# Kernel optimization log

Hardware: AMD Instinct MI355X
Metric: run time of the kernel (lower is better)

## Reference

```python
import jax, jax.numpy as jnp
import numpy as np

B, OBS, ACT, NT, E = 4096, 512, 64, 10, 16
DREP, DH, DK = 1024, 1024, 512  # rep dim, expert hidden, key/value dim


def setup_inputs() -> dict:
    key = jax.random.key(0)
    ks = jax.random.split(key, 24)
    s = 0.02
    state_core = jax.random.normal(ks[0], (B, OBS), jnp.float32)
    task_ids = jax.random.randint(ks[1], (B,), 0, NT)
    onehot = jax.nn.one_hot(task_ids, NT, dtype=jnp.float32)
    state = jnp.concatenate([state_core, onehot], axis=-1)  # [B, OBS+NT]
    act = jax.random.normal(ks[2], (B, ACT), jnp.float32)
    return {
        "state": state,
        "act": act,
        "rep_W0": s * jax.random.normal(ks[3], (OBS + ACT, DREP), jnp.float32),
        "rep_b0": jnp.zeros((DREP,), jnp.float32),
        "rep_W1": s * jax.random.normal(ks[4], (DREP, DREP), jnp.float32),
        "rep_b1": jnp.zeros((DREP,), jnp.float32),
        "emb": 0.5 * jnp.ones((NT, DK), jnp.float32),
        "Wk0": s * jax.random.normal(ks[5], (E, DREP, DH), jnp.float32),
        "bk0": jnp.zeros((E, DH), jnp.float32),
        "Wk1": s * jax.random.normal(ks[6], (E, DH, DK), jnp.float32),
        "bk1": jnp.zeros((E, DK), jnp.float32),
        "Wv0": s * jax.random.normal(ks[7], (E, DREP, DH), jnp.float32),
        "bv0": jnp.zeros((E, DH), jnp.float32),
        "Wv1": s * jax.random.normal(ks[8], (E, DH, DK), jnp.float32),
        "bv1": jnp.zeros((E, DK), jnp.float32),
        "Wt0": s * jax.random.normal(ks[9], (DK, 512), jnp.float32),
        "bt0": jnp.zeros((512,), jnp.float32),
        "Wt1": s * jax.random.normal(ks[10], (512, 256), jnp.float32),
        "bt1": jnp.zeros((256,), jnp.float32),
        "Wt2": s * jax.random.normal(ks[11], (256, 1), jnp.float32),
        "bt2": jnp.zeros((1,), jnp.float32),
    }


def reference(state, act, rep_W0, rep_b0, rep_W1, rep_b1, emb,
              Wk0, bk0, Wk1, bk1, Wv0, bv0, Wv1, bv1,
              Wt0, bt0, Wt1, bt1, Wt2, bt2):
    num_tasks = emb.shape[0]
    task = jnp.argmax(state[:, -num_tasks:], axis=-1)  # one-hot -> index (== torch.nonzero)
    s = state[:, :-num_tasks]
    # representation: mlp([obs+act, 1024, 1024]) -> relu then identity
    x = jnp.concatenate([s, act], axis=-1)
    rep = jax.nn.relu(x @ rep_W0 + rep_b0) @ rep_W1 + rep_b1  # [B, DREP]
    query = jnp.tanh(emb[task])  # [B, DK]
    # all experts batched (original loops in Python over E tiny MLPs)
    hk = jax.nn.relu(jnp.einsum('bd,edh->ebh', rep, Wk0) + bk0[:, None, :])
    keys = jnp.einsum('ebh,ehk->ebk', hk, Wk1) + bk1[:, None, :]   # [E,B,DK]
    hv = jax.nn.relu(jnp.einsum('bd,edh->ebh', rep, Wv0) + bv0[:, None, :])
    vals = jnp.einsum('ebh,ehk->ebk', hv, Wv1) + bv1[:, None, :]   # [E,B,DK]
    logits = jnp.einsum('bk,ebk->be', query, keys)                 # [B,E]
    attn = jax.nn.softmax(logits, axis=1)
    tower_in = jnp.einsum('be,ebk->bk', attn, vals)                # [B,DK]
    h = jax.nn.relu(tower_in @ Wt0 + bt0)
    h = jax.nn.relu(h @ Wt1 + bt1)
    q = jnp.squeeze(h @ Wt2 + bt2, -1)                             # [B]
    expert_loss = -jnp.mean(
        jnp.sum(jnp.clip(jnp.log(attn + 1e-10), -6.0, 0.0), axis=-1) * 0.3)
    return q, expert_loss
```

## Files before the change

kernel.cpp:

```cpp
#include <hip/hip_runtime.h>
#include <cstdint>
#include <cstddef>

#define NB   4096
#define OBS  512
#define NACT 64
#define NT   10
#define NE   16
#define DREP 1024
#define DH   1024
#define DK   512
#define SLD  (OBS + NT)
#define XK   (OBS + NACT)

typedef short s8v __attribute__((ext_vector_type(8)));
typedef float f4v __attribute__((ext_vector_type(4)));

__device__ __forceinline__ unsigned short f2bf(float f) {
  union { float f; unsigned int u; } v; v.f = f;
  unsigned int u = v.u;
  unsigned int r = (u + 0x7FFFu + ((u >> 16) & 1u)) >> 16;
  return (unsigned short)r;
}
__device__ __forceinline__ float bf2f(unsigned short h) {
  union { unsigned int u; float f; } v; v.u = ((unsigned int)h) << 16;
  return v.f;
}

__device__ __forceinline__ void gload_lds16(const unsigned short* gp, const unsigned short* lp) {
  __builtin_amdgcn_global_load_lds(
      (const __attribute__((address_space(1))) void*)(uintptr_t)gp,
      (__attribute__((address_space(3))) void*)(unsigned int)(uintptr_t)lp,
      16, 0, 0);
}

template <int BM, int BN, int MODE, int RELU, int LDA, int LDB, int KK>
__global__ void __launch_bounds__(256)
gemm_k(const unsigned short* __restrict__ A,
       const unsigned short* __restrict__ Bt,
       const float* __restrict__ bias,
       unsigned short* __restrict__ outB, int ldo,
       const float* __restrict__ qk1, const int* __restrict__ task,
       float* __restrict__ logits, int eBase,
       const float* __restrict__ attn, float* __restrict__ cio)
{
  constexpr int FM = BM / 32;
  constexpr int FN = BN / 32;
  constexpr int CA = BM / 64;
  constexpr int CB = BN / 64;
  constexpr int NTILES = KK / 32;
  static_assert(NTILES >= 3, "pipeline depth");
  constexpr int LPS = CA + CB;
  static_assert(LPS < 16, "vmcnt immediate fits in low bits");
  constexpr int WAIT_STAGE = 0xF70 | LPS;
  constexpr int WAIT_ALL   = 0xF70;

  __shared__ __align__(16) unsigned short As[3][BM * 32];
  __shared__ __align__(16) unsigned short Bs[3][BN * 32];

  const int tid  = threadIdx.x;
  const int wave = tid >> 6;
  const int lane = tid & 63;
  const int wm = wave >> 1, wn = wave & 1;

  const int rowBase = blockIdx.x * BM;
  const int colBase = blockIdx.y * BN;

  int eg = 0;
  if (MODE == 1) {
    eg = blockIdx.z;
    Bt  += (size_t)eg * (DREP * DH);
    bias += eg * DH;
    qk1 += (size_t)eg * (NT * DH);
  }
  if (MODE == 2) {
    eg = eBase + blockIdx.z;
    Bt  += (size_t)eg * (DREP * DH);
    bias += eg * DH;
    outB += (size_t)blockIdx.z * DH;
  }
  if (MODE == 3 || MODE == 4) {
    A   += (size_t)blockIdx.z * KK;
    Bt  += (size_t)blockIdx.z * KK;
    cio += (size_t)blockIdx.z * NB * DK;
  }

  f4v acc[FM][FN];
#pragma unroll
  for (int m = 0; m < FM; ++m)
#pragma unroll
    for (int n = 0; n < FN; ++n) acc[m][n] = f4v{0.f, 0.f, 0.f, 0.f};

  const int sRow = lane >> 2;
  const int sSw  = ((lane & 3) ^ ((sRow >> 1) & 3)) * 8;

  const unsigned short* ag[CA];
  const unsigned short* bg[CB];
#pragma unroll
  for (int j = 0; j < CA; ++j)
    ag[j] = A + (size_t)(rowBase + (wave * CA + j) * 16 + sRow) * LDA + sSw;
#pragma unroll
  for (int j = 0; j < CB; ++j)
    bg[j] = Bt + (size_t)(colBase + (wave * CB + j) * 16 + sRow) * LDB + sSw;

  const int fr   = lane & 15;
  const int koSw = ((lane >> 4) ^ ((fr >> 1) & 3)) * 8;
  const int aOff = (wm * (BM / 2) + fr) * 32 + koSw;
  const int bOff = (wn * (BN / 2) + fr) * 32 + koSw;

  auto stage = [&](int buf) {
#pragma unroll
    for (int j = 0; j < CA; ++j) { gload_lds16(ag[j], &As[buf][(wave * CA + j) * 512]); ag[j] += 32; }
#pragma unroll
    for (int j = 0; j < CB; ++j) { gload_lds16(bg[j], &Bs[buf][(wave * CB + j) * 512]); bg[j] += 32; }
  };

  auto compute = [&](int buf) {
    s8v av[FM], bv[FN];
#pragma unroll
    for (int m = 0; m < FM; ++m)
      av[m] = *reinterpret_cast<const s8v*>(&As[buf][aOff + m * 512]);
#pragma unroll
    for (int n = 0; n < FN; ++n)
      bv[n] = *reinterpret_cast<const s8v*>(&Bs[buf][bOff + n * 512]);
#pragma unroll
    for (int m = 0; m < FM; ++m)
#pragma unroll
      for (int n = 0; n < FN; ++n)
        acc[m][n] = __builtin_amdgcn_mfma_f32_16x16x32_bf16(av[m], bv[n], acc[m][n], 0, 0, 0);
  };

  stage(0);
  stage(1);

  for (int t = 0; t < NTILES; t += 3) {
    if (t + 1 < NTILES) __builtin_amdgcn_s_waitcnt(WAIT_STAGE);
    else                __builtin_amdgcn_s_waitcnt(WAIT_ALL);
    __builtin_amdgcn_s_barrier();
    if (t + 2 < NTILES) stage(2);
    compute(0);
    if (t + 1 < NTILES) {
      if (t + 2 < NTILES) __builtin_amdgcn_s_waitcnt(WAIT_STAGE);
      else                __builtin_amdgcn_s_waitcnt(WAIT_ALL);
      __builtin_amdgcn_s_barrier();
      if (t + 3 < NTILES) stage(0);
      compute(1);
    }
    if (t + 2 < NTILES) {
      if (t + 3 < NTILES) __builtin_amdgcn_s_waitcnt(WAIT_STAGE);
      else                __builtin_amdgcn_s_waitcnt(WAIT_ALL);
      __builtin_amdgcn_s_barrier();
      if (t + 4 < NTILES) stage(1);
      compute(2);
    }
  }

  const int cr = (lane >> 4) * 4;
  const int cc = lane & 15;

  int gcn[FN];
  float bcol[FN];
#pragma unroll
  for (int n = 0; n < FN; ++n) {
    gcn[n] = colBase + wn * (BN / 2) + n * 16 + cc;
    bcol[n] = (MODE >= 3) ? 0.f : bias[gcn[n]];
  }

  if (MODE == 0 || MODE == 2) {
#pragma unroll
    for (int m = 0; m < FM; ++m)
#pragma unroll
      for (int r = 0; r < 4; ++r) {
        int gr = rowBase + wm * (BM / 2) + m * 16 + cr + r;
        float aw = 1.f;
        if (MODE == 2) aw = attn[gr * NE + eg];
#pragma unroll
        for (int n = 0; n < FN; ++n) {
          float v = acc[m][n][r] + bcol[n];
          if (RELU) v = fmaxf(v, 0.f);
          if (MODE == 2) v *= aw;
          outB[(size_t)gr * ldo + gcn[n]] = f2bf(v);
        }
      }
  }

  if (MODE == 1) {
#pragma unroll
    for (int m = 0; m < FM; ++m)
#pragma unroll
      for (int r = 0; r < 4; ++r) {
        int gr = rowBase + wm * (BM / 2) + m * 16 + cr + r;
        int tk = task[gr];
        const float* qrow = qk1 + (size_t)tk * DH;
        float s = 0.f;
#pragma unroll
        for (int n = 0; n < FN; ++n) {
          float v = fmaxf(acc[m][n][r] + bcol[n], 0.f);
          s += v * qrow[gcn[n]];
        }
#pragma unroll
        for (int off = 1; off < 16; off <<= 1) s += __shfl_xor(s, off, 64);
        if (cc == 0) atomicAdd(&logits[gr * NE + eg], s);
      }
  }

  if (MODE == 3 || MODE == 4) {
#pragma unroll
    for (int m = 0; m < FM; ++m)
#pragma unroll
      for (int r = 0; r < 4; ++r) {
        int gr = rowBase + wm * (BM / 2) + m * 16 + cr + r;
#pragma unroll
        for (int n = 0; n < FN; ++n) {
          float v = acc[m][n][r];
          if (MODE == 4) v += cio[(size_t)gr * DK + gcn[n]];
          cio[(size_t)gr * DK + gcn[n]] = v;
        }
      }
  }
}

__global__ void task_k(const float* __restrict__ state, int* __restrict__ task) {
  int b = blockIdx.x * blockDim.x + threadIdx.x;
  if (b >= NB) return;
  const float* p = state + (size_t)b * SLD + OBS;
  float best = p[0]; int bi = 0;
  for (int j = 1; j < NT; ++j) { float v = p[j]; if (v > best) { best = v; bi = j; } }
  task[b] = bi;
}

__global__ void buildx_k(const float* __restrict__ state, const float* __restrict__ act,
                         unsigned short* __restrict__ x) {
  int idx = blockIdx.x * blockDim.x + threadIdx.x;
  if (idx >= NB * XK) return;
  int b = idx / XK, j = idx - b * XK;
  float v = (j < OBS) ? state[(size_t)b * SLD + j] : act[(size_t)b * NACT + (j - OBS)];
  x[idx] = f2bf(v);
}

__global__ void prep_emb_k(const float* __restrict__ emb, const float* __restrict__ bk1,
                           float* __restrict__ Qt, float* __restrict__ qb) {
  int t = blockIdx.x;
  __shared__ float qsh[DK];
  for (int k = threadIdx.x; k < DK; k += 256) {
    float v = tanhf(emb[t * DK + k]);
    Qt[t * DK + k] = v;
    qsh[k] = v;
  }
  __syncthreads();
  int wave = threadIdx.x >> 6, lane = threadIdx.x & 63;
  for (int e = wave; e < NE; e += 4) {
    float s = 0.f;
    for (int k = lane; k < DK; k += 64) s += qsh[k] * bk1[e * DK + k];
    for (int off = 1; off < 64; off <<= 1) s += __shfl_xor(s, off, 64);
    if (lane == 0) qb[e * NT + t] = s;
  }
}

__global__ void qk1_k(const float* __restrict__ Wk1, const float* __restrict__ Qt,
                      float* __restrict__ qk1) {
  int w = (blockIdx.x * blockDim.x + threadIdx.x) >> 6;
  int lane = threadIdx.x & 63;
  if (w >= NE * DH) return;
  int e = w >> 10, h = w & (DH - 1);
  const float* wrow = Wk1 + ((size_t)e * DH + h) * DK + lane * 8;
  float wv[8];
#pragma unroll
  for (int j = 0; j < 8; ++j) wv[j] = wrow[j];
#pragma unroll
  for (int t = 0; t < NT; ++t) {
    const float* qrow = Qt + t * DK + lane * 8;
    float s = 0.f;
#pragma unroll
    for (int j = 0; j < 8; ++j) s += wv[j] * qrow[j];
#pragma unroll
    for (int off = 1; off < 64; off <<= 1) s += __shfl_xor(s, off, 64);
    if (lane == 0) qk1[((size_t)e * NT + t) * DH + h] = s;
  }
}

__global__ void __launch_bounds__(256)
convT_k(const float* __restrict__ src, unsigned short* __restrict__ dst,
        int N, long sBS, long dBS, int dLd) {
  __shared__ float tile[64][65];
  int e = blockIdx.z;
  int n0 = blockIdx.x * 64, k0 = blockIdx.y * 64;
  src += (size_t)e * sBS + (size_t)k0 * N + n0;
  dst += (size_t)e * dBS + (size_t)n0 * dLd + k0;
  int t = threadIdx.x;
  int c4 = t & 15, kr = t >> 4;
#pragma unroll
  for (int i = 0; i < 4; ++i) {
    float4 v = *(const float4*)(src + (size_t)(kr + i * 16) * N + c4 * 4);
    tile[kr + i * 16][c4 * 4 + 0] = v.x;
    tile[kr + i * 16][c4 * 4 + 1] = v.y;
    tile[kr + i * 16][c4 * 4 + 2] = v.z;
    tile[kr + i * 16][c4 * 4 + 3] = v.w;
  }
  __syncthreads();
  int sub = t & 7, nl = t >> 3;
#pragma unroll
  for (int pass = 0; pass < 2; ++pass) {
    int n = nl + pass * 32;
    unsigned short v8[8];
#pragma unroll
    for (int j = 0; j < 8; ++j) v8[j] = f2bf(tile[sub * 8 + j][n]);
    *reinterpret_cast<s8v*>(dst + (size_t)n * dLd + sub * 8) =
        *reinterpret_cast<const s8v*>(v8);
  }
}

__global__ void softmax_k(const float* __restrict__ logits, const float* __restrict__ qb,
                          const int* __restrict__ task, float* __restrict__ attn,
                          float* __restrict__ lossOut) {
  int b = blockIdx.x * blockDim.x + threadIdx.x;
  int t = task[b];
  float l[NE];
  float mx = -1e30f;
#pragma unroll
  for (int e = 0; e < NE; ++e) { l[e] = logits[b * NE + e] + qb[e * NT + t]; mx = fmaxf(mx, l[e]); }
  float s = 0.f;
#pragma unroll
  for (int e = 0; e < NE; ++e) { l[e] = expf(l[e] - mx); s += l[e]; }
  float inv = 1.f / s;
  float loss = 0.f;
#pragma unroll
  for (int e = 0; e < NE; ++e) {
    float a = l[e] * inv;
    attn[b * NE + e] = a;
    float lg = logf(a + 1e-10f);
    loss += fminf(fmaxf(lg, -6.f), 0.f);
  }
  for (int off = 1; off < 64; off <<= 1) loss += __shfl_xor(loss, off, 64);
  if ((threadIdx.x & 63) == 0) atomicAdd(lossOut, loss * (-0.3f / NB));
}

__global__ void towerbias_k(const float* __restrict__ attn, const float* __restrict__ bv1,
                            float* __restrict__ towerin) {
  int idx = blockIdx.x * blockDim.x + threadIdx.x;
  if (idx >= NB * DK) return;
  int b = idx >> 9, k = idx & (DK - 1);
  float s = 0.f;
#pragma unroll
  for (int e = 0; e < NE; ++e) s += attn[b * NE + e] * bv1[e * DK + k];
  towerin[idx] = s;
}

__global__ void cvt_ti_k(const float* __restrict__ twin, const float* __restrict__ P,
                         unsigned short* __restrict__ ti) {
  int idx = (blockIdx.x * blockDim.x + threadIdx.x) * 8;
  if (idx >= NB * DK) return;
  float v[8];
#pragma unroll
  for (int j = 0; j < 8; ++j) v[j] = twin[idx + j];
#pragma unroll
  for (int c = 0; c < 4; ++c) {
    const float* p = P + (size_t)c * NB * DK + idx;
#pragma unroll
    for (int j = 0; j < 8; ++j) v[j] += p[j];
  }
  unsigned short v8[8];
#pragma unroll
  for (int j = 0; j < 8; ++j) v8[j] = f2bf(v[j]);
  *reinterpret_cast<s8v*>(ti + idx) = *reinterpret_cast<const s8v*>(v8);
}

__global__ void qfinal_k(const unsigned short* __restrict__ h2, const float* __restrict__ Wt2,
                         const float* __restrict__ bt2, float* __restrict__ out) {
  int w = (blockIdx.x * blockDim.x + threadIdx.x) >> 6;
  int lane = threadIdx.x & 63;
  if (w >= NB) return;
  float s = 0.f;
#pragma unroll
  for (int j = 0; j < 4; ++j) {
    int k = lane * 4 + j;
    s += bf2f(h2[(size_t)w * 256 + k]) * Wt2[k];
  }
  for (int off = 1; off < 64; off <<= 1) s += __shfl_xor(s, off, 64);
  if (lane == 0) out[w] = s + bt2[0];
}

extern "C" void kernel_launch(void* const* d_in, const int* in_sizes, int n_in,
                              void* d_out, int out_size, void* d_ws, size_t ws_size,
                              hipStream_t stream) {
  const float* state  = (const float*)d_in[0];
  const float* act    = (const float*)d_in[1];
  const float* rep_W0 = (const float*)d_in[2];
  const float* rep_b0 = (const float*)d_in[3];
  const float* rep_W1 = (const float*)d_in[4];
  const float* rep_b1 = (const float*)d_in[5];
  const float* emb    = (const float*)d_in[6];
  const float* Wk0    = (const float*)d_in[7];
  const float* bk0    = (const float*)d_in[8];
  const float* Wk1    = (const float*)d_in[9];
  const float* bk1    = (const float*)d_in[10];
  const float* Wv0    = (const float*)d_in[11];
  const float* bv0    = (const float*)d_in[12];
  const float* Wv1    = (const float*)d_in[13];
  const float* bv1    = (const float*)d_in[14];
  const float* Wt0    = (const float*)d_in[15];
  const float* bt0    = (const float*)d_in[16];
  const float* Wt1    = (const float*)d_in[17];
  const float* bt1    = (const float*)d_in[18];
  const float* Wt2    = (const float*)d_in[19];
  const float* bt2    = (const float*)d_in[20];
  float* out = (float*)d_out;

  char* wsb = (char*)d_ws;
  size_t off = 0;
  auto alloc = [&](size_t bytes) -> void* {
    void* p = wsb + off;
    off += (bytes + 255) & ~(size_t)255;
    return p;
  };
  unsigned short* Ap    = (unsigned short*)alloc((size_t)NB * 8192 * 2);
  unsigned short* Wk0t  = (unsigned short*)alloc((size_t)NE * DREP * DH * 2);
  unsigned short* Wv0t  = (unsigned short*)alloc((size_t)NE * DREP * DH * 2);
  unsigned short* Wv1t  = (unsigned short*)alloc((size_t)DK * (NE * DH) * 2);
  float*          P     = (float*)alloc((size_t)4 * NB * DK * 4);
  unsigned short* h0    = (unsigned short*)alloc((size_t)NB * DREP * 2);
  unsigned short* rep   = (unsigned short*)alloc((size_t)NB * DREP * 2);
  float*          twin  = (float*)alloc((size_t)NB * DK * 4);
  unsigned short* xbuf  = (unsigned short*)alloc((size_t)NB * XK * 2);
  unsigned short* ti    = (unsigned short*)alloc((size_t)NB * DK * 2);
  unsigned short* h1    = (unsigned short*)alloc((size_t)NB * 512 * 2);
  unsigned short* h2    = (unsigned short*)alloc((size_t)NB * 256 * 2);
  unsigned short* rW1t  = (unsigned short*)alloc((size_t)DREP * DREP * 2);
  unsigned short* rW0t  = (unsigned short*)alloc((size_t)DREP * XK * 2);
  float*          qk1   = (float*)alloc((size_t)NE * NT * DH * 4);
  unsigned short* Wt0t  = (unsigned short*)alloc((size_t)512 * 512 * 2);
  unsigned short* Wt1t  = (unsigned short*)alloc((size_t)256 * 512 * 2);
  float*          logits= (float*)alloc((size_t)NB * NE * 4);
  float*          attn  = (float*)alloc((size_t)NB * NE * 4);
  float*          Qt    = (float*)alloc((size_t)NT * DK * 4);
  int*            task  = (int*)alloc((size_t)NB * 4);
  float*          qb    = (float*)alloc((size_t)NE * NT * 4);

  hipMemsetAsync(logits, 0, (size_t)NB * NE * 4, stream);
  hipMemsetAsync(out + NB, 0, sizeof(float), stream);

  task_k<<<NB / 256, 256, 0, stream>>>(state, task);
  buildx_k<<<(NB * XK + 255) / 256, 256, 0, stream>>>(state, act, xbuf);
  prep_emb_k<<<NT, 256, 0, stream>>>(emb, bk1, Qt, qb);
  qk1_k<<<NE * DH / 4, 256, 0, stream>>>(Wk1, Qt, qk1);

  convT_k<<<dim3(DREP / 64, XK / 64, 1), 256, 0, stream>>>(rep_W0, rW0t, DREP, 0, 0, XK);
  convT_k<<<dim3(DREP / 64, DREP / 64, 1), 256, 0, stream>>>(rep_W1, rW1t, DREP, 0, 0, DREP);
  convT_k<<<dim3(DH / 64, DREP / 64, NE), 256, 0, stream>>>(Wk0, Wk0t, DH, (long)DREP * DH, (long)DREP * DH, DREP);
  convT_k<<<dim3(DH / 64, DREP / 64, NE), 256, 0, stream>>>(Wv0, Wv0t, DH, (long)DREP * DH, (long)DREP * DH, DREP);
  convT_k<<<dim3(DK / 64, DH / 64, NE), 256, 0, stream>>>(Wv1, Wv1t, DK, (long)DH * DK, 1024L, NE * DH);
  convT_k<<<dim3(512 / 64, 512 / 64, 1), 256, 0, stream>>>(Wt0, Wt0t, 512, 0, 0, 512);
  convT_k<<<dim3(256 / 64, 512 / 64, 1), 256, 0, stream>>>(Wt1, Wt1t, 256, 0, 0, 512);

  gemm_k<128, 128, 0, 1, XK, XK, XK><<<dim3(NB / 128, DREP / 128, 1), 256, 0, stream>>>(
      xbuf, rW0t, rep_b0, h0, DREP, nullptr, nullptr, nullptr, 0, nullptr, nullptr);
  gemm_k<128, 128, 0, 0, DREP, DREP, DREP><<<dim3(NB / 128, DREP / 128, 1), 256, 0, stream>>>(
      h0, rW1t, rep_b1, rep, DREP, nullptr, nullptr, nullptr, 0, nullptr, nullptr);

  gemm_k<128, 128, 1, 1, DREP, DREP, DREP><<<dim3(NB / 128, DH / 128, NE), 256, 0, stream>>>(
      rep, Wk0t, bk0, nullptr, 0, qk1, task, logits, 0, nullptr, nullptr);

  softmax_k<<<NB / 256, 256, 0, stream>>>(logits, qb, task, attn, out + NB);
  towerbias_k<<<NB * DK / 256, 256, 0, stream>>>(attn, bv1, twin);

  for (int g = 0; g < 2; ++g) {
    gemm_k<128, 128, 2, 1, DREP, DREP, DREP><<<dim3(NB / 128, DH / 128, 8), 256, 0, stream>>>(
        rep, Wv0t, bv0, Ap, 8192, nullptr, nullptr, nullptr, g * 8, attn, nullptr);
    if (g == 0)
      gemm_k<128, 128, 3, 0, 8192, NE * DH, 2048><<<dim3(NB / 128, DK / 128, 4), 256, 0, stream>>>(
          Ap, Wv1t, nullptr, nullptr, 0, nullptr, nullptr, nullptr, 0, nullptr, P);
    else
      gemm_k<128, 128, 4, 0, 8192, NE * DH, 2048><<<dim3(NB / 128, DK / 128, 4), 256, 0, stream>>>(
          Ap, Wv1t + (size_t)8192, nullptr, nullptr, 0, nullptr, nullptr, nullptr, 0, nullptr, P);
  }
  cvt_ti_k<<<(NB * DK / 8 + 255) / 256, 256, 0, stream>>>(twin, P, ti);

  gemm_k<64, 64, 0, 1, DK, DK, DK><<<dim3(NB / 64, 512 / 64, 1), 256, 0, stream>>>(
      ti, Wt0t, bt0, h1, 512, nullptr, nullptr, nullptr, 0, nullptr, nullptr);
  gemm_k<64, 64, 0, 1, 512, 512, 512><<<dim3(NB / 64, 256 / 64, 1), 256, 0, stream>>>(
      h1, Wt1t, bt1, h2, 256, nullptr, nullptr, nullptr, 0, nullptr, nullptr);
  qfinal_k<<<NB / 4, 256, 0, stream>>>(h2, Wt2, bt2, out);
}
```

Before: 780.1 us.

## Add 256x256-tile 8-wave GEMM kernel for expert key/value first layers

Introduces a new GEMM kernel with 256x256 output tiles, 512 threads, and K-step 64, using double-buffered LDS staging interleaved across four quadrant MFMA blocks with setprio. The expert Wk0 (logit-fused) and Wv0 (attn-scaled) GEMMs, the dominant FLOP cost, move to it, while the old 128x128 kernel drops those modes. Larger tiles double operand reuse per LDS load and cut global traffic, at the cost of 128KB LDS per block, fewer blocks per CU, and a more intricate barrier and waitcnt schedule.

```diff
diff --git a/kernel.cpp b/kernel.cpp
--- a/kernel.cpp
+++ b/kernel.cpp
@@ -66,19 +66,6 @@
   const int rowBase = blockIdx.x * BM;
   const int colBase = blockIdx.y * BN;
 
-  int eg = 0;
-  if (MODE == 1) {
-    eg = blockIdx.z;
-    Bt  += (size_t)eg * (DREP * DH);
-    bias += eg * DH;
-    qk1 += (size_t)eg * (NT * DH);
-  }
-  if (MODE == 2) {
-    eg = eBase + blockIdx.z;
-    Bt  += (size_t)eg * (DREP * DH);
-    bias += eg * DH;
-    outB += (size_t)blockIdx.z * DH;
-  }
   if (MODE == 3 || MODE == 4) {
     A   += (size_t)blockIdx.z * KK;
     Bt  += (size_t)blockIdx.z * KK;
@@ -166,41 +153,18 @@
     bcol[n] = (MODE >= 3) ? 0.f : bias[gcn[n]];
   }
 
-  if (MODE == 0 || MODE == 2) {
+  if (MODE == 0) {
 #pragma unroll
     for (int m = 0; m < FM; ++m)
 #pragma unroll
       for (int r = 0; r < 4; ++r) {
         int gr = rowBase + wm * (BM / 2) + m * 16 + cr + r;
-        float aw = 1.f;
-        if (MODE == 2) aw = attn[gr * NE + eg];
 #pragma unroll
         for (int n = 0; n < FN; ++n) {
           float v = acc[m][n][r] + bcol[n];
           if (RELU) v = fmaxf(v, 0.f);
-          if (MODE == 2) v *= aw;
           outB[(size_t)gr * ldo + gcn[n]] = f2bf(v);
         }
-      }
-  }
-
-  if (MODE == 1) {
-#pragma unroll
-    for (int m = 0; m < FM; ++m)
-#pragma unroll
-      for (int r = 0; r < 4; ++r) {
-        int gr = rowBase + wm * (BM / 2) + m * 16 + cr + r;
-        int tk = task[gr];
-        const float* qrow = qk1 + (size_t)tk * DH;
-        float s = 0.f;
-#pragma unroll
-        for (int n = 0; n < FN; ++n) {
-          float v = fmaxf(acc[m][n][r] + bcol[n], 0.f);
-          s += v * qrow[gcn[n]];
-        }
-#pragma unroll
-        for (int off = 1; off < 16; off <<= 1) s += __shfl_xor(s, off, 64);
-        if (cc == 0) atomicAdd(&logits[gr * NE + eg], s);
       }
   }
 
@@ -217,6 +181,199 @@
           cio[(size_t)gr * DK + gcn[n]] = v;
         }
       }
+  }
+}
+
+template <int MODE, int LDA, int LDB, int KK>
+__global__ void __launch_bounds__(512)
+gemm256_k(const unsigned short* __restrict__ A,
+          const unsigned short* __restrict__ Bt,
+          const float* __restrict__ bias,
+          unsigned short* __restrict__ outB, int ldo,
+          const float* __restrict__ qk1, const int* __restrict__ task,
+          float* __restrict__ logits, int eBase,
+          const float* __restrict__ attn)
+{
+  constexpr int NTK = KK / 64;
+  static_assert(NTK >= 4 && (NTK & 1) == 0, "pipeline depth");
+
+  __shared__ __align__(16) unsigned short As[2][16384];
+  __shared__ __align__(16) unsigned short Bs[2][16384];
+
+  const int tid  = threadIdx.x;
+  const int wave = tid >> 6;
+  const int lane = tid & 63;
+
+  const int rowBase = blockIdx.x * 256;
+  const int colBase = blockIdx.y * 256;
+
+  int eg = 0;
+  if (MODE == 1) {
+    eg = blockIdx.z;
+    Bt   += (size_t)eg * ((size_t)DREP * DH);
+    bias += eg * DH;
+    qk1  += (size_t)eg * (NT * DH);
+  }
+  if (MODE == 2) {
+    eg = eBase + blockIdx.z;
+    Bt   += (size_t)eg * ((size_t)DREP * DH);
+    bias += eg * DH;
+    outB += (size_t)blockIdx.z * DH;
+  }
+
+  f4v acc[2][2][2][4];
+#pragma unroll
+  for (int i0 = 0; i0 < 2; ++i0)
+#pragma unroll
+    for (int i1 = 0; i1 < 2; ++i1)
+#pragma unroll
+      for (int i2 = 0; i2 < 2; ++i2)
+#pragma unroll
+        for (int i3 = 0; i3 < 4; ++i3)
+          acc[i0][i1][i2][i3] = f4v{0.f, 0.f, 0.f, 0.f};
+
+  const int l3 = lane >> 3, l7 = lane & 7, l4 = lane >> 4;
+  size_t srcA[2], srcB[2];
+#pragma unroll
+  for (int j = 0; j < 2; ++j) {
+    const int r  = j * 64 + wave * 8 + l3;
+    const int ks = (l7 ^ l3) * 8;
+    srcA[j] = (size_t)(rowBase + r) * LDA + ks;
+    srcB[j] = (size_t)(colBase + r) * LDB + ks;
+  }
+
+  auto stageA = [&](int buf, int half, int t) {
+#pragma unroll
+    for (int j = 0; j < 2; ++j)
+      gload_lds16(A + srcA[j] + (size_t)half * (128 * LDA) + t * 64,
+                  &As[buf][half * 8192 + j * 4096 + wave * 512]);
+  };
+  auto stageB = [&](int buf, int half, int t) {
+#pragma unroll
+    for (int j = 0; j < 2; ++j)
+      gload_lds16(Bt + srcB[j] + (size_t)half * (128 * LDB) + t * 64,
+                  &Bs[buf][half * 8192 + j * 4096 + wave * 512]);
+  };
+
+  const int cOff0 = (l4 ^ l7) * 8;
+  const int cOff1 = ((4 + l4) ^ l7) * 8;
+  const int aRowOff = ((wave & 3) * 32 + (lane & 15)) * 64;
+  const int bColOff = ((wave >> 2) * 64 + (lane & 15)) * 64;
+
+  s8v av[2][2], bv[4][2];
+  auto readA = [&](int buf, int qm) {
+#pragma unroll
+    for (int f = 0; f < 2; ++f) {
+      const unsigned short* p = &As[buf][qm * 8192 + aRowOff + f * 1024];
+      av[f][0] = *reinterpret_cast<const s8v*>(p + cOff0);
+      av[f][1] = *reinterpret_cast<const s8v*>(p + cOff1);
+    }
+  };
+  auto readB = [&](int buf, int qn) {
+#pragma unroll
+    for (int fc = 0; fc < 4; ++fc) {
+      const unsigned short* p = &Bs[buf][qn * 8192 + bColOff + fc * 1024];
+      bv[fc][0] = *reinterpret_cast<const s8v*>(p + cOff0);
+      bv[fc][1] = *reinterpret_cast<const s8v*>(p + cOff1);
+    }
+  };
+
+#define MFMA_BLK(QM, QN)                                                      \
+  do {                                                                        \
+    __builtin_amdgcn_s_setprio(1);                                            \
+    _Pragma("unroll") for (int ks_ = 0; ks_ < 2; ++ks_)                       \
+      _Pragma("unroll") for (int f_ = 0; f_ < 2; ++f_)                        \
+        _Pragma("unroll") for (int fc_ = 0; fc_ < 4; ++fc_)                   \
+          acc[QM][QN][f_][fc_] = __builtin_amdgcn_mfma_f32_16x16x32_bf16(     \
+              av[f_][ks_], bv[fc_][ks_], acc[QM][QN][f_][fc_], 0, 0, 0);      \
+    __builtin_amdgcn_s_setprio(0);                                            \
+  } while (0)
+
+  stageA(0, 0, 0); stageB(0, 0, 0); stageA(0, 1, 0); stageB(0, 1, 0);
+  stageB(1, 0, 1); stageA(1, 1, 1);
+  __builtin_amdgcn_s_waitcnt(0xF74);
+  __builtin_amdgcn_s_barrier();
+
+  for (int t = 0; t < NTK; ++t) {
+    const int buf = t & 1;
+    readA(buf, 0); readB(buf, 0);
+    if (t + 1 < NTK) stageA(buf ^ 1, 0, t + 1);
+    __builtin_amdgcn_s_barrier();
+    MFMA_BLK(0, 0);
+    __builtin_amdgcn_s_barrier();
+    readA(buf, 1);
+    if (t + 1 < NTK) stageB(buf ^ 1, 1, t + 1);
+    __builtin_amdgcn_s_barrier();
+    MFMA_BLK(1, 0);
+    __builtin_amdgcn_s_barrier();
+    readB(buf, 1);
+    if (t + 2 < NTK) stageB(buf, 0, t + 2);
+    __builtin_amdgcn_s_barrier();
+    MFMA_BLK(1, 1);
+    __builtin_amdgcn_s_barrier();
+    readA(buf, 0);
+    if (t + 2 < NTK) stageA(buf, 1, t + 2);
+    if (t + 2 < NTK)      __builtin_amdgcn_s_waitcnt(0xF74);
+    else if (t + 1 < NTK) __builtin_amdgcn_s_waitcnt(0xF70);
+    __builtin_amdgcn_s_barrier();
+    MFMA_BLK(0, 1);
+    __builtin_amdgcn_s_barrier();
+  }
+#undef MFMA_BLK
+
+  const int cr = l4 * 4;
+  const int cc = lane & 15;
+
+  int gcn[2][4];
+  float bcol[2][4];
+#pragma unroll
+  for (int qn = 0; qn < 2; ++qn)
+#pragma unroll
+    for (int fc = 0; fc < 4; ++fc) {
+      gcn[qn][fc]  = colBase + qn * 128 + (wave >> 2) * 64 + fc * 16 + cc;
+      bcol[qn][fc] = bias[gcn[qn][fc]];
+    }
+
+  if (MODE == 1) {
+#pragma unroll
+    for (int qm = 0; qm < 2; ++qm)
+#pragma unroll
+      for (int f = 0; f < 2; ++f)
+#pragma unroll
+        for (int r = 0; r < 4; ++r) {
+          const int gr = rowBase + qm * 128 + (wave & 3) * 32 + f * 16 + cr + r;
+          const float* qrow = qk1 + (size_t)task[gr] * DH;
+          float s = 0.f;
+#pragma unroll
+          for (int qn = 0; qn < 2; ++qn)
+#pragma unroll
+            for (int fc = 0; fc < 4; ++fc) {
+              float v = fmaxf(acc[qm][qn][f][fc][r] + bcol[qn][fc], 0.f);
+              s += v * qrow[gcn[qn][fc]];
+            }
+#pragma unroll
+          for (int off = 1; off < 16; off <<= 1) s += __shfl_xor(s, off, 64);
+          if (cc == 0) atomicAdd(&logits[gr * NE + eg], s);
+        }
+  }
+
+  if (MODE == 2) {
+#pragma unroll
+    for (int qm = 0; qm < 2; ++qm)
+#pragma unroll
+      for (int f = 0; f < 2; ++f)
+#pragma unroll
+        for (int r = 0; r < 4; ++r) {
+          const int gr = rowBase + qm * 128 + (wave & 3) * 32 + f * 16 + cr + r;
+          const float aw = attn[gr * NE + eg];
+#pragma unroll
+          for (int qn = 0; qn < 2; ++qn)
+#pragma unroll
+            for (int fc = 0; fc < 4; ++fc) {
+              float v = fmaxf(acc[qm][qn][f][fc][r] + bcol[qn][fc], 0.f) * aw;
+              outB[(size_t)gr * ldo + gcn[qn][fc]] = f2bf(v);
+            }
+        }
   }
 }
 
@@ -457,15 +614,15 @@
   gemm_k<128, 128, 0, 0, DREP, DREP, DREP><<<dim3(NB / 128, DREP / 128, 1), 256, 0, stream>>>(
       h0, rW1t, rep_b1, rep, DREP, nullptr, nullptr, nullptr, 0, nullptr, nullptr);
 
-  gemm_k<128, 128, 1, 1, DREP, DREP, DREP><<<dim3(NB / 128, DH / 128, NE), 256, 0, stream>>>(
-      rep, Wk0t, bk0, nullptr, 0, qk1, task, logits, 0, nullptr, nullptr);
+  gemm256_k<1, DREP, DREP, DREP><<<dim3(NB / 256, DH / 256, NE), 512, 0, stream>>>(
+      rep, Wk0t, bk0, nullptr, 0, qk1, task, logits, 0, nullptr);
 
   softmax_k<<<NB / 256, 256, 0, stream>>>(logits, qb, task, attn, out + NB);
   towerbias_k<<<NB * DK / 256, 256, 0, stream>>>(attn, bv1, twin);
 
   for (int g = 0; g < 2; ++g) {
-    gemm_k<128, 128, 2, 1, DREP, DREP, DREP><<<dim3(NB / 128, DH / 128, 8), 256, 0, stream>>>(
-        rep, Wv0t, bv0, Ap, 8192, nullptr, nullptr, nullptr, g * 8, attn, nullptr);
+    gemm256_k<2, DREP, DREP, DREP><<<dim3(NB / 256, DH / 256, 8), 512, 0, stream>>>(
+        rep, Wv0t, bv0, Ap, 8192, nullptr, nullptr, nullptr, g * 8, attn);
     if (g == 0)
       gemm_k<128, 128, 3, 0, 8192, NE * DH, 2048><<<dim3(NB / 128, DK / 128, 4), 256, 0, stream>>>(
           Ap, Wv1t, nullptr, nullptr, 0, nullptr, nullptr, nullptr, 0, nullptr, P);
```

Result: faster. 746.1 us (-4.3%).

## Add 256x256-tile 8-wave GEMM kernel for per-expert key/value first layers

Applied to the files above, without the earlier changes.

Adds a new GEMM kernel with 256x256 output tiles, 512 threads (8 waves), a triple-buffered LDS pipeline split into two MFMA half-phases, and an XCD-aware workgroup remapping of the flat block index. The two largest per-expert GEMMs (key layer with fused logit reduction, value layer with fused attention scaling) now use it, while their epilogues are removed from the generic kernel. Larger tiles raise arithmetic intensity and cut redundant global/LDS traffic. The cost is higher register and LDS pressure (48 KB per buffer set pair) and fewer blocks in flight.

```diff
diff --git a/kernel.cpp b/kernel.cpp
--- a/kernel.cpp
+++ b/kernel.cpp
@@ -66,19 +66,6 @@
   const int rowBase = blockIdx.x * BM;
   const int colBase = blockIdx.y * BN;
 
-  int eg = 0;
-  if (MODE == 1) {
-    eg = blockIdx.z;
-    Bt  += (size_t)eg * (DREP * DH);
-    bias += eg * DH;
-    qk1 += (size_t)eg * (NT * DH);
-  }
-  if (MODE == 2) {
-    eg = eBase + blockIdx.z;
-    Bt  += (size_t)eg * (DREP * DH);
-    bias += eg * DH;
-    outB += (size_t)blockIdx.z * DH;
-  }
   if (MODE == 3 || MODE == 4) {
     A   += (size_t)blockIdx.z * KK;
     Bt  += (size_t)blockIdx.z * KK;
@@ -166,41 +153,18 @@
     bcol[n] = (MODE >= 3) ? 0.f : bias[gcn[n]];
   }
 
-  if (MODE == 0 || MODE == 2) {
+  if (MODE == 0) {
 #pragma unroll
     for (int m = 0; m < FM; ++m)
 #pragma unroll
       for (int r = 0; r < 4; ++r) {
         int gr = rowBase + wm * (BM / 2) + m * 16 + cr + r;
-        float aw = 1.f;
-        if (MODE == 2) aw = attn[gr * NE + eg];
 #pragma unroll
         for (int n = 0; n < FN; ++n) {
           float v = acc[m][n][r] + bcol[n];
           if (RELU) v = fmaxf(v, 0.f);
-          if (MODE == 2) v *= aw;
           outB[(size_t)gr * ldo + gcn[n]] = f2bf(v);
         }
-      }
-  }
-
-  if (MODE == 1) {
-#pragma unroll
-    for (int m = 0; m < FM; ++m)
-#pragma unroll
-      for (int r = 0; r < 4; ++r) {
-        int gr = rowBase + wm * (BM / 2) + m * 16 + cr + r;
-        int tk = task[gr];
-        const float* qrow = qk1 + (size_t)tk * DH;
-        float s = 0.f;
-#pragma unroll
-        for (int n = 0; n < FN; ++n) {
-          float v = fmaxf(acc[m][n][r] + bcol[n], 0.f);
-          s += v * qrow[gcn[n]];
-        }
-#pragma unroll
-        for (int off = 1; off < 16; off <<= 1) s += __shfl_xor(s, off, 64);
-        if (cc == 0) atomicAdd(&logits[gr * NE + eg], s);
       }
   }
 
@@ -217,6 +181,191 @@
           cio[(size_t)gr * DK + gcn[n]] = v;
         }
       }
+  }
+}
+
+template <int MODE, int LDA, int LDB, int KK>
+__global__ void __launch_bounds__(512)
+gemm256_k(const unsigned short* __restrict__ A,
+          const unsigned short* __restrict__ Bt,
+          const float* __restrict__ bias,
+          unsigned short* __restrict__ outB, int ldo,
+          const float* __restrict__ qk1, const int* __restrict__ task,
+          float* __restrict__ logits, int eBase,
+          const float* __restrict__ attn)
+{
+  constexpr int NTK = KK / 32;
+  static_assert(NTK >= 4, "pipeline depth");
+  constexpr int BUFS = 8192;
+
+  __shared__ __align__(16) unsigned short AsF[3 * BUFS];
+  __shared__ __align__(16) unsigned short BsF[3 * BUFS];
+
+  const int tid  = threadIdx.x;
+  const int wave = tid >> 6;
+  const int lane = tid & 63;
+  const int fr = lane & 15;
+  const int l4 = lane >> 4;
+  const int wave_m = wave >> 2;
+  const int wave_n = wave & 3;
+
+  const int gx = gridDim.x, gy = gridDim.y;
+  int flat = blockIdx.x + gx * (blockIdx.y + gy * blockIdx.z);
+  const int nwg = gx * gy * gridDim.z;
+  flat = (flat & 7) * (nwg >> 3) + (flat >> 3);
+  const int bx = flat % gx; flat /= gx;
+  const int by = flat % gy;
+  const int bz = flat / gy;
+
+  const int rowBase = bx * 256;
+  const int colBase = by * 256;
+
+  int eg = 0;
+  if (MODE == 1) {
+    eg = bz;
+    Bt   += (size_t)eg * ((size_t)DREP * DH);
+    bias += eg * DH;
+    qk1  += (size_t)eg * (NT * DH);
+  }
+  if (MODE == 2) {
+    eg = eBase + bz;
+    Bt   += (size_t)eg * ((size_t)DREP * DH);
+    bias += eg * DH;
+    outB += (size_t)bz * DH;
+  }
+
+  f4v acc[2][4][4];
+#pragma unroll
+  for (int i0 = 0; i0 < 2; ++i0)
+#pragma unroll
+    for (int i1 = 0; i1 < 4; ++i1)
+#pragma unroll
+      for (int i2 = 0; i2 < 4; ++i2)
+        acc[i0][i1][i2] = f4v{0.f, 0.f, 0.f, 0.f};
+
+  const int sRow = lane >> 2;
+  const int sKo  = ((lane & 3) ^ (sRow & 3)) * 8;
+  const unsigned short* pA[2];
+  const unsigned short* pB[2];
+#pragma unroll
+  for (int h = 0; h < 2; ++h) {
+    const int r = h * 128 + wave * 16 + sRow;
+    pA[h] = A  + (size_t)(rowBase + r) * LDA + sKo;
+    pB[h] = Bt + (size_t)(colBase + r) * LDB + sKo;
+  }
+
+  auto stageA = [&](int bufO, int h) {
+    gload_lds16(pA[h], &AsF[bufO + h * 4096 + wave * 512]);
+    pA[h] += 32;
+  };
+  auto stageB = [&](int bufO, int h) {
+    gload_lds16(pB[h], &BsF[bufO + h * 4096 + wave * 512]);
+    pB[h] += 32;
+  };
+
+  const int swz   = (l4 ^ (fr & 3)) * 8;
+  const int aC    = wave_m * 4096 + fr * 32 + swz;
+  const int bC    = (wave_n >> 1) * 4096 + ((wave_n & 1) * 64 + fr) * 32 + swz;
+
+  s8v av[4], bv[4];
+  auto readA = [&](int aAddr, int rh) {
+#pragma unroll
+    for (int m4 = 0; m4 < 4; ++m4)
+      av[m4] = *reinterpret_cast<const s8v*>(&AsF[aAddr + rh * 2048 + m4 * 512]);
+  };
+  auto readB = [&](int bAddr) {
+#pragma unroll
+    for (int n4 = 0; n4 < 4; ++n4)
+      bv[n4] = *reinterpret_cast<const s8v*>(&BsF[bAddr + n4 * 512]);
+  };
+
+#define MFMA_PH(RH)                                                           \
+  do {                                                                        \
+    __builtin_amdgcn_s_setprio(1);                                            \
+    _Pragma("unroll") for (int m4_ = 0; m4_ < 4; ++m4_)                       \
+      _Pragma("unroll") for (int n4_ = 0; n4_ < 4; ++n4_)                     \
+        acc[RH][m4_][n4_] = __builtin_amdgcn_mfma_f32_16x16x32_bf16(          \
+            av[m4_], bv[n4_], acc[RH][m4_][n4_], 0, 0, 0);                    \
+    __builtin_amdgcn_s_setprio(0);                                            \
+  } while (0)
+
+  stageA(0, 0); stageA(0, 1); stageB(0, 0); stageB(0, 1);
+  stageA(BUFS, 0); stageA(BUFS, 1); stageB(BUFS, 0); stageB(BUFS, 1);
+  __builtin_amdgcn_s_waitcnt(0xF74);
+  __builtin_amdgcn_s_barrier();
+
+  int bufR = 0;
+  int bufS = 2 * BUFS;
+
+  for (int t = 0; t < NTK; ++t) {
+    const bool st = (t + 2) < NTK;
+    const int aAddr = bufR + aC;
+    const int bAddr = bufR + bC;
+    readA(aAddr, 0);
+    readB(bAddr);
+    if (st) { stageA(bufS, 0); stageA(bufS, 1); }
+    __builtin_amdgcn_s_barrier();
+    MFMA_PH(0);
+    __builtin_amdgcn_s_barrier();
+    readA(aAddr, 1);
+    if (st) { stageB(bufS, 0); stageB(bufS, 1); }
+    if (st)               __builtin_amdgcn_s_waitcnt(0xF74);
+    else if (t + 1 < NTK) __builtin_amdgcn_s_waitcnt(0xF70);
+    __builtin_amdgcn_s_barrier();
+    MFMA_PH(1);
+    __builtin_amdgcn_s_barrier();
+    bufR = (bufR == 2 * BUFS) ? 0 : bufR + BUFS;
+    bufS = (bufS == 2 * BUFS) ? 0 : bufS + BUFS;
+  }
+#undef MFMA_PH
+
+  const int cr = l4 * 4;
+  const int cc = fr;
+
+  int gcn[4];
+  float bcol[4];
+#pragma unroll
+  for (int n4 = 0; n4 < 4; ++n4) {
+    gcn[n4]  = colBase + wave_n * 64 + n4 * 16 + cc;
+    bcol[n4] = bias[gcn[n4]];
+  }
+
+  if (MODE == 1) {
+#pragma unroll
+    for (int rh = 0; rh < 2; ++rh)
+#pragma unroll
+      for (int m4 = 0; m4 < 4; ++m4)
+#pragma unroll
+        for (int r = 0; r < 4; ++r) {
+          const int gr = rowBase + wave_m * 128 + rh * 64 + m4 * 16 + cr + r;
+          const float* qrow = qk1 + (size_t)task[gr] * DH;
+          float s = 0.f;
+#pragma unroll
+          for (int n4 = 0; n4 < 4; ++n4) {
+            float v = fmaxf(acc[rh][m4][n4][r] + bcol[n4], 0.f);
+            s += v * qrow[gcn[n4]];
+          }
+#pragma unroll
+          for (int off = 1; off < 16; off <<= 1) s += __shfl_xor(s, off, 64);
+          if (cc == 0) atomicAdd(&logits[gr * NE + eg], s);
+        }
+  }
+
+  if (MODE == 2) {
+#pragma unroll
+    for (int rh = 0; rh < 2; ++rh)
+#pragma unroll
+      for (int m4 = 0; m4 < 4; ++m4)
+#pragma unroll
+        for (int r = 0; r < 4; ++r) {
+          const int gr = rowBase + wave_m * 128 + rh * 64 + m4 * 16 + cr + r;
+          const float aw = attn[gr * NE + eg];
+#pragma unroll
+          for (int n4 = 0; n4 < 4; ++n4) {
+            float v = fmaxf(acc[rh][m4][n4][r] + bcol[n4], 0.f) * aw;
+            outB[(size_t)gr * ldo + gcn[n4]] = f2bf(v);
+          }
+        }
   }
 }
 
@@ -457,15 +606,15 @@
   gemm_k<128, 128, 0, 0, DREP, DREP, DREP><<<dim3(NB / 128, DREP / 128, 1), 256, 0, stream>>>(
       h0, rW1t, rep_b1, rep, DREP, nullptr, nullptr, nullptr, 0, nullptr, nullptr);
 
-  gemm_k<128, 128, 1, 1, DREP, DREP, DREP><<<dim3(NB / 128, DH / 128, NE), 256, 0, stream>>>(
-      rep, Wk0t, bk0, nullptr, 0, qk1, task, logits, 0, nullptr, nullptr);
+  gemm256_k<1, DREP, DREP, DREP><<<dim3(NB / 256, DH / 256, NE), 512, 0, stream>>>(
+      rep, Wk0t, bk0, nullptr, 0, qk1, task, logits, 0, nullptr);
 
   softmax_k<<<NB / 256, 256, 0, stream>>>(logits, qb, task, attn, out + NB);
   towerbias_k<<<NB * DK / 256, 256, 0, stream>>>(attn, bv1, twin);
 
   for (int g = 0; g < 2; ++g) {
-    gemm_k<128, 128, 2, 1, DREP, DREP, DREP><<<dim3(NB / 128, DH / 128, 8), 256, 0, stream>>>(
-        rep, Wv0t, bv0, Ap, 8192, nullptr, nullptr, nullptr, g * 8, attn, nullptr);
+    gemm256_k<2, DREP, DREP, DREP><<<dim3(NB / 256, DH / 256, 8), 512, 0, stream>>>(
+        rep, Wv0t, bv0, Ap, 8192, nullptr, nullptr, nullptr, g * 8, attn);
     if (g == 0)
       gemm_k<128, 128, 3, 0, 8192, NE * DH, 2048><<<dim3(NB / 128, DK / 128, 4), 256, 0, stream>>>(
           Ap, Wv1t, nullptr, nullptr, 0, nullptr, nullptr, nullptr, 0, nullptr, P);
```

Result: slower. 818.0 us (+4.9%).
